# Kernel tuning notes

Hardware: AMD Instinct MI355X
Metric: run time of the kernel (lower is better)

Reference implementation:

```python
import jax, jax.numpy as jnp
import numpy as np

E = 768      # embedding_dim == hidden_dim (required for shape consistency)
U = 256      # number of utterances in the dialogue
NSPK = 8     # number of distinct speakers
SCALE = 0.03 # ~ torch's uniform(-1/sqrt(H), 1/sqrt(H)) init magnitude


def _p(k, shape):
    return jax.random.normal(k, shape, dtype=jnp.float32) * SCALE


def setup_inputs() -> dict:
    key = jax.random.key(0)
    ks = jax.random.split(key, 32)
    d = {}
    d["dialogue"] = jax.random.normal(ks[0], (U, E), dtype=jnp.float32)
    d["speakers"] = jax.random.randint(ks[1], (U,), 0, NSPK)
    # attention linears (stored [in, out], applied as x @ W + b)
    d["Wq"] = _p(ks[2], (E, E));      d["bq"] = _p(ks[3], (E,))
    d["Wk"] = _p(ks[4], (2 * E, E));  d["bk"] = _p(ks[5], (E,))
    d["Wv"] = _p(ks[6], (E, E));      d["bv"] = _p(ks[7], (E,))
    # speaker_GRU: input 2E, hidden E, bidirectional (torch layout [3H, in]/[3H, H])
    d["sWih_f"] = _p(ks[8], (3 * E, 2 * E)); d["sWhh_f"] = _p(ks[9], (3 * E, E))
    d["sbih_f"] = _p(ks[10], (3 * E,));      d["sbhh_f"] = _p(ks[11], (3 * E,))
    d["sWih_b"] = _p(ks[12], (3 * E, 2 * E)); d["sWhh_b"] = _p(ks[13], (3 * E, E))
    d["sbih_b"] = _p(ks[14], (3 * E,));       d["sbhh_b"] = _p(ks[15], (3 * E,))
    # global_GRU: input 3E, hidden E, bidirectional
    d["gWih_f"] = _p(ks[16], (3 * E, 3 * E)); d["gWhh_f"] = _p(ks[17], (3 * E, E))
    d["gbih_f"] = _p(ks[18], (3 * E,));       d["gbhh_f"] = _p(ks[19], (3 * E,))
    d["gWih_b"] = _p(ks[20], (3 * E, 3 * E)); d["gWhh_b"] = _p(ks[21], (3 * E, E))
    d["gbih_b"] = _p(ks[22], (3 * E,));       d["gbhh_b"] = _p(ks[23], (3 * E,))
    # random initial states, as in the original forward
    d["h0_global"] = jax.random.normal(ks[24], (2, E), dtype=jnp.float32)
    d["h0_speaker"] = jax.random.normal(ks[25], (2, E), dtype=jnp.float32)
    d["att0"] = jax.random.normal(ks[26], (E,), dtype=jnp.float32)
    return d


def _gru_cell(x, h, Wih, Whh, bih, bhh):
    # torch GRUCell math; gate order r, z, n
    gx = Wih @ x + bih
    gh = Whh @ h + bhh
    H = h.shape[0]
    r = jax.nn.sigmoid(gx[:H] + gh[:H])
    z = jax.nn.sigmoid(gx[H:2 * H] + gh[H:2 * H])
    n = jnp.tanh(gx[2 * H:] + r * gh[2 * H:])
    return (1.0 - z) * n + z * h


def reference(dialogue, speakers, Wq, bq, Wk, bk, Wv, bv,
              sWih_f, sWhh_f, sbih_f, sbhh_f, sWih_b, sWhh_b, sbih_b, sbhh_b,
              gWih_f, gWhh_f, gbih_f, gbhh_f, gWih_b, gWhh_b, gbih_b, gbhh_b,
              h0_global, h0_speaker, att0):
    Ul, El = dialogue.shape
    norm = jnp.sqrt(jnp.float32(El))
    pos = jnp.arange(Ul)
    sstates0 = jnp.broadcast_to(h0_speaker, (NSPK, 2, El))  # every speaker starts at h0_speaker
    buf0 = jnp.zeros((Ul, 2 * El), dtype=dialogue.dtype)    # global_output buffer

    def step(carry, xs):
        buf, gh, sst = carry
        u, sp, t = xs
        sh = sst[sp]  # [2, E] speaker hidden (fwd/bwd)
        # attention over global_output[:t+1] (row t is still zeros, as in torch)
        q = u @ Wq + bq                       # [E]
        k = buf @ Wk + bk                     # [U, E]
        v = k @ Wv + bv                       # [U, E] (note: w_v applied to projected key, as in source)
        score = (k @ q) / norm                # [U]
        score = jnp.where(pos <= t, score, jnp.float32(-1e9))
        att = jax.nn.softmax(score) @ v       # [E]
        att = jnp.where(t == 0, att0, att)    # t==0 uses random initial attention output
        tmp = jnp.concatenate([att, u])       # [2E]
        hf = _gru_cell(tmp, sh[0], sWih_f, sWhh_f, sbih_f, sbhh_f)
        hb = _gru_cell(tmp, sh[1], sWih_b, sWhh_b, sbih_b, sbhh_b)
        so = jnp.concatenate([hf, hb]) + tmp  # speaker_output[t] = GRU out + residual tmp
        sst = sst.at[sp].set(jnp.stack([hf, hb]))
        fop = jnp.concatenate([so, u])        # [3E]
        gf = _gru_cell(fop, gh[0], gWih_f, gWhh_f, gbih_f, gbhh_f)
        gb = _gru_cell(fop, gh[1], gWih_b, gWhh_b, gbih_b, gbhh_b)
        buf = buf.at[t].set(jnp.concatenate([gf, gb]))
        return (buf, jnp.stack([gf, gb]), sst), so

    (buf, _, _), so_seq = jax.lax.scan(step, (buf0, h0_global, sstates0),
                                       (dialogue, speakers, pos))
    return buf, so_seq  # (global_output [U,2E], speaker_output [U,2E])
```

## Files before the change

kernel.cpp:

```cpp
#include <hip/hip_runtime.h>
#include <hip/hip_bf16.h>

#define E_ 768
#define E2_ 1536
#define E3_ 2304
#define U_ 256
#define NORM_ 27.712812921102035f
#define NREP 16

typedef unsigned int u32;
typedef unsigned long long u64;

__device__ __align__(16) float g_Q[U_ * E_];
__device__ __align__(16) float g_WQg[U_ * E2_];
__device__ __align__(16) float g_WKVT[E_ * E2_];
__device__ __align__(16) float g_vb[E_];
__device__ int g_run;

__device__ __align__(64) u64 g_mb_bg[NREP * U_ * 8];
__device__ __align__(64) u64 g_mb_so[NREP * U_ * 8];
__device__ __align__(64) u64 g_mb_h [2 * NREP * U_ * 8 * 4];
__device__ __align__(64) u64 g_mb_sc[2 * NREP * U_];

__device__ __forceinline__ float bflo(u32 v){ return __uint_as_float(v << 16); }
__device__ __forceinline__ float bfhi(u32 v){ return __uint_as_float(v & 0xffff0000u); }

__device__ __forceinline__ u32 packbf(float lo, float hi){
  u32 a = __float_as_uint(lo), b = __float_as_uint(hi);
  a = (a + 0x7FFFu + ((a >> 16) & 1u)) >> 16;
  b = (b + 0x7FFFu + ((b >> 16) & 1u)) & 0xFFFF0000u;
  return (a & 0xFFFFu) | b;
}
__device__ __forceinline__ unsigned short bfr(float x){
  u32 a = __float_as_uint(x);
  return (unsigned short)((a + 0x7FFFu + ((a >> 16) & 1u)) >> 16);
}

__device__ __forceinline__ u64 aload64(const u64* p){
  return __hip_atomic_load(p, __ATOMIC_RELAXED, __HIP_MEMORY_SCOPE_AGENT);
}
__device__ __forceinline__ void astore64(u64* p, u64 v){
  __hip_atomic_store(p, v, __ATOMIC_RELAXED, __HIP_MEMORY_SCOPE_AGENT);
}
__device__ __forceinline__ u64 pk(float f, u32 tag){ return (u64)__float_as_uint(f) | ((u64)tag << 32); }
__device__ __forceinline__ float pf(u64 v){ return __uint_as_float((u32)v); }
__device__ __forceinline__ u32 ptag(u64 v){ return (u32)(v >> 32); }

__device__ __forceinline__ void bar_lds(){
  asm volatile("s_waitcnt lgkmcnt(0)\n\ts_barrier" ::: "memory");
}

__device__ __forceinline__ float wsum(float v){
#pragma unroll
  for (int o = 32; o > 0; o >>= 1) v += __shfl_xor(v, o, 64);
  return v;
}
__device__ __forceinline__ float wmax(float v){
#pragma unroll
  for (int o = 32; o > 0; o >>= 1) v = fmaxf(v, __shfl_xor(v, o, 64));
  return v;
}

__global__ __launch_bounds__(256) void init_kernel(const float* bk, const float* Wv,
                                                   const float* bv)
{
  __shared__ float acc4[4][64];
  int tid = threadIdx.x;
  if (blockIdx.x == 0 && tid == 0) g_run = g_run + 1;
  int b = blockIdx.x;
  int o = b * 64 + (tid & 63);
  int w = tid >> 6;
  float s = 0.f;
  for (int i2 = w * 192; i2 < w * 192 + 192; ++i2)
    s = fmaf(bk[i2], Wv[(size_t)i2 * E_ + o], s);
  acc4[w][tid & 63] = s;
  __syncthreads();
  if (w == 0)
    g_vb[o] = acc4[0][tid & 63] + acc4[1][tid & 63] + acc4[2][tid & 63] + acc4[3][tid & 63] + bv[o];
}

template<int ASRC, int BNK, int DST, int TC>
__global__ __launch_bounds__(256) void gemm32(const float* __restrict__ Aext, int lda,
                                              const float* __restrict__ B, int ldb,
                                              const float* __restrict__ bias, float scale,
                                              int ldc, int M, int N, int K)
{
  const float* A = (ASRC == 1) ? g_Q : Aext;
  float* C = (DST == 0) ? g_Q : (DST == 1) ? g_WQg : g_WKVT;
  __shared__ float As[64][17];
  __shared__ float Bs[16][65];
  int tid = threadIdx.x;
  int tx = tid & 15, ty = tid >> 4;
  int m0 = blockIdx.y * 64, n0 = blockIdx.x * 64;
  float acc[4][4] = {{0.f}};
  for (int k0 = 0; k0 < K; k0 += 16) {
#pragma unroll
    for (int i = 0; i < 4; ++i) {
      int li = tid + 256 * i;
      int m = li >> 4, kk = li & 15;
      As[m][kk] = A[(size_t)(m0 + m) * lda + k0 + kk];
    }
#pragma unroll
    for (int i = 0; i < 4; ++i) {
      int li = tid + 256 * i;
      if (BNK) {
        int n = li >> 4, kk = li & 15;
        Bs[kk][n] = B[(size_t)(n0 + n) * ldb + k0 + kk];
      } else {
        int kk = li >> 6, n = li & 63;
        Bs[kk][n] = B[(size_t)(k0 + kk) * ldb + n0 + n];
      }
    }
    __syncthreads();
#pragma unroll
    for (int kk = 0; kk < 16; ++kk) {
      float av[4], bv4[4];
#pragma unroll
      for (int i = 0; i < 4; ++i) av[i] = As[ty * 4 + i][kk];
#pragma unroll
      for (int j = 0; j < 4; ++j) bv4[j] = Bs[kk][tx * 4 + j];
#pragma unroll
      for (int i = 0; i < 4; ++i)
#pragma unroll
        for (int j = 0; j < 4; ++j) acc[i][j] = fmaf(av[i], bv4[j], acc[i][j]);
    }
    __syncthreads();
  }
#pragma unroll
  for (int i = 0; i < 4; ++i)
#pragma unroll
    for (int j = 0; j < 4; ++j) {
      int m = m0 + ty * 4 + i, n = n0 + tx * 4 + j;
      float c = acc[i][j] * scale;
      if (bias) c += bias[n];
      if (TC) C[(size_t)n * ldc + m] = c;
      else    C[(size_t)m * ldc + n] = c;
    }
}

struct SeqArgs {
  const float *dialogue, *sWih_f, *sWih_b, *sWhh_f, *sWhh_b,
      *sbih_f, *sbih_b, *sbhh_f, *sbhh_b,
      *gWih_f, *gWih_b, *gWhh_f, *gWhh_b, *gbih_f, *gbih_b, *gbhh_f, *gbhh_b,
      *att0, *h0g, *h0s;
  const int* speakers;
  float* out;
};

__global__ __launch_bounds__(256, 1) void seq_kernel(SeqArgs a)
{
  const int tid = threadIdx.x, wg = blockIdx.x;
  const int wave = tid >> 6, lane = tid & 63;
  const int h0 = wg * 3;
  const int myrep = wg & (NREP - 1);

  __shared__ float wsa[18][768];
  __shared__ float wkv_lds[3][E2_];
  __shared__ float M_l[18][U_];
  __shared__ float ghrow[E2_];
  __shared__ float bufc[E2_];
  __shared__ float hv[E2_];
  __shared__ float so_f[E2_];
  __shared__ float V_lds[U_][3];
  __shared__ float e_lds[U_];
  __shared__ float ghs_s[18], ghg_s[18], sxu[18], gxu[18], gxs[18], mcol[18];
  __shared__ float Mvb_l[18], A0_l[18];
  __shared__ float red4[4], red4b[4], pmax[4], pnum[4][4], att_s[3];
  __shared__ float pub12[12], pubbg[6];
  __shared__ float hloc[8][6];
  __shared__ float ghloc[6];
  __shared__ int spk_l[U_], locc_l[U_], pocc_l[U_];

  for (int idx = tid; idx < 18 * 768; idx += 256) {
    int r = idx / 768, e = idx - r * 768;
    int dir = r / 9, lr = r - dir * 9, g = lr / 3, d = lr - g * 3;
    int gr = g * E_ + h0 + d;
    const float* pa = (dir ? a.sWih_b : a.sWih_f) + (size_t)gr * E2_;
    wsa[r][e] = pa[e];
  }
  for (int idx = tid; idx < 3 * E2_; idx += 256) {
    int r = idx / E2_, k = idx - r * E2_;
    wkv_lds[r][k] = g_WKVT[(size_t)(h0 + r) * E2_ + k];
  }
  spk_l[tid] = a.speakers[tid] & 7;
  __syncthreads();
  {
    int mysp = spk_l[tid], lo = -1, cnt = 0;
    for (int s2 = 0; s2 <= tid; ++s2)
      if (spk_l[s2] == mysp) { cnt++; if (s2 < tid) lo = s2; }
    locc_l[tid] = lo;
    pocc_l[tid] = cnt & 1;
  }
#pragma unroll
  for (int q = 0; q < 5; ++q) {
    int sr = wave + 4 * q;
    if (sr < 18) {
      float s0 = 0.f, s1 = 0.f;
#pragma unroll
      for (int pp = 0; pp < 12; ++pp) {
        int e = lane + 64 * pp;
        float w = wsa[sr][e];
        s0 = fmaf(w, g_vb[e], s0);
        s1 = fmaf(w, a.att0[e], s1);
      }
      s0 = wsum(s0); s1 = wsum(s1);
      if (lane == 0) { Mvb_l[sr] = s0; A0_l[sr] = s1; }
    }
  }
  __syncthreads();
  for (int half = 0; half < 2; ++half) {
    float acc[9][6];
#pragma unroll
    for (int r = 0; r < 9; ++r)
#pragma unroll
      for (int c = 0; c < 6; ++c) acc[r][c] = 0.f;
    for (int e = 0; e < 768; e += 2) {
      const float* B0 = g_WKVT + (size_t)e * E2_ + tid;
      const float* B1 = B0 + E2_;
      float b0[6], b1[6];
#pragma unroll
      for (int c = 0; c < 6; ++c) { b0[c] = B0[256 * c]; b1[c] = B1[256 * c]; }
#pragma unroll
      for (int r = 0; r < 9; ++r) {
        float2 w = ((const float2*)wsa[half * 9 + r])[e >> 1];
#pragma unroll
        for (int c = 0; c < 6; ++c)
          acc[r][c] = fmaf(w.x, b0[c], fmaf(w.y, b1[c], acc[r][c]));
      }
    }
    __syncthreads();
    unsigned short* wsp = (unsigned short*)wsa;
#pragma unroll
    for (int r = 0; r < 9; ++r)
#pragma unroll
      for (int c = 0; c < 6; ++c)
        wsp[(half * 9 + r) * 1536 + tid + 256 * c] = bfr(acc[r][c]);
    __syncthreads();
  }
  const u32* wsp32 = (const u32*)wsa;

  u32 wSU[5][6], wSHH[5][6], wGHH[5][6], wGSO[5][12], wGU[5][6];
  float bSH[5], bGH[5], bSI[5], bGI[5];
#pragma unroll
  for (int q = 0; q < 5; ++q) {
    int sr = wave + 4 * q;
    if (sr < 18) {
      int dir = sr / 9, lr = sr - dir * 9, g = lr / 3, d = lr - g * 3;
      int gr = g * E_ + h0 + d;
      const float* pa  = (dir ? a.sWih_b : a.sWih_f) + (size_t)gr * E2_;
      const float* ph  = (dir ? a.sWhh_b : a.sWhh_f) + (size_t)gr * E_;
      const float* pgs = (dir ? a.gWih_b : a.gWih_f) + (size_t)gr * E3_;
      const float* pgh = (dir ? a.gWhh_b : a.gWhh_f) + (size_t)gr * E_;
#pragma unroll
      for (int pp = 0; pp < 6; ++pp) {
        int j2 = 2 * (lane + 64 * pp);
        wSU[q][pp]  = packbf(pa[768 + j2], pa[768 + j2 + 1]);
        wSHH[q][pp] = packbf(ph[j2], ph[j2 + 1]);
        wGHH[q][pp] = packbf(pgh[j2], pgh[j2 + 1]);
        wGU[q][pp]  = packbf(pgs[1536 + j2], pgs[1536 + j2 + 1]);
      }
#pragma unroll
      for (int pp = 0; pp < 12; ++pp) {
        int j2 = 2 * (lane + 64 * pp);
        wGSO[q][pp] = packbf(pgs[j2], pgs[j2 + 1]);
      }
      bSH[q] = (dir ? a.sbhh_b : a.sbhh_f)[gr];
      bSI[q] = (dir ? a.sbih_b : a.sbih_f)[gr];
      bGH[q] = (dir ? a.gbhh_b : a.gbhh_f)[gr];
      bGI[q] = (dir ? a.gbih_b : a.gbih_f)[gr];
    }
  }
  const float vb0 = g_vb[h0], vb1 = g_vb[h0 + 1], vb2 = g_vb[h0 + 2];
  if (tid < 6) ghloc[tid] = a.h0g[(tid / 3) * E_ + h0 + (tid % 3)];
  __syncthreads();

  const u32 rb = ((u32)g_run) << 9;

  for (int t = 0; t < U_; ++t) {
    const int sp = spk_l[t];
    const int locc = locc_l[t];
    const u32 tagT = rb + (u32)t;
    const float2* uv = (const float2*)(a.dialogue + (size_t)t * E_);

#pragma unroll
    for (int q = 0; q < 5; ++q) {
      int sr = wave + 4 * q;
      if (sr < 18) {
        float s3 = 0.f, s4 = 0.f;
#pragma unroll
        for (int pp = 0; pp < 6; ++pp) {
          int j = lane + 64 * pp;
          u32 v3 = wSU[q][pp], v4 = wGU[q][pp];
          float2 xu = uv[j];
          s3 = fmaf(bflo(v3), xu.x, s3); s3 = fmaf(bfhi(v3), xu.y, s3);
          s4 = fmaf(bflo(v4), xu.x, s4); s4 = fmaf(bfhi(v4), xu.y, s4);
        }
        s3 = wsum(s3); s4 = wsum(s4);
        if (lane == 0) { sxu[sr] = s3 + bSI[q]; gxu[sr] = s4 + bGI[q]; }
      }
    }

    float slp = 0.f;
    if (t == 0) {
      for (int i = tid; i < E2_; i += 256) ghrow[i] = a.h0g[i];
    } else {
      const u64* p = &g_mb_bg[((size_t)myrep * U_ + tid) * 8];
      u64 x0 = aload64(p), x1 = aload64(p + 1), x2 = aload64(p + 2);
      const u32 exp = rb + (u32)(t - 1);
      for (;;) {
        bool ok = (ptag(x0) == exp) & (ptag(x1) == exp) & (ptag(x2) == exp);
        if (ok) break;
        if (ptag(x0) != exp) x0 = aload64(p);
        if (ptag(x1) != exp) x1 = aload64(p + 1);
        if (ptag(x2) != exp) x2 = aload64(p + 2);
      }
      u32 w0 = (u32)x0, w1 = (u32)x1, w2 = (u32)x2;
      float f0 = bflo(w0), f1 = bfhi(w0), f2 = bflo(w1);
      float f3 = bfhi(w1), f4 = bflo(w2), f5 = bfhi(w2);
      ghrow[3 * tid]          = f0;
      ghrow[3 * tid + 1]      = f1;
      ghrow[3 * tid + 2]      = f2;
      ghrow[E_ + 3 * tid]     = f3;
      ghrow[E_ + 3 * tid + 1] = f4;
      ghrow[E_ + 3 * tid + 2] = f5;
      if (wg == t - 1) {
        bufc[3 * tid]          = f0;
        bufc[3 * tid + 1]      = f1;
        bufc[3 * tid + 2]      = f2;
        bufc[E_ + 3 * tid]     = f3;
        bufc[E_ + 3 * tid + 1] = f4;
        bufc[E_ + 3 * tid + 2] = f5;
      }
      const float* wq = g_WQg + (size_t)t * E2_;
      slp = f0 * wq[3 * tid] + f1 * wq[3 * tid + 1] + f2 * wq[3 * tid + 2]
          + f3 * wq[E_ + 3 * tid] + f4 * wq[E_ + 3 * tid + 1] + f5 * wq[E_ + 3 * tid + 2];
    }
    if (locc >= 0) {
      const int spar = pocc_l[t] ^ 1;
      const u64* p = &g_mb_h[((((size_t)spar * NREP + myrep) * U_ + tid) * 8 + sp) * 4];
      u64 x0 = aload64(p), x1 = aload64(p + 1), x2 = aload64(p + 2);
      const u32 exp = rb + (u32)locc;
      for (;;) {
        bool ok = (ptag(x0) == exp) & (ptag(x1) == exp) & (ptag(x2) == exp);
        if (ok) break;
        if (ptag(x0) != exp) x0 = aload64(p);
        if (ptag(x1) != exp) x1 = aload64(p + 1);
        if (ptag(x2) != exp) x2 = aload64(p + 2);
      }
      u32 w0 = (u32)x0, w1 = (u32)x1, w2 = (u32)x2;
      hv[3 * tid]          = bflo(w0);
      hv[3 * tid + 1]      = bfhi(w0);
      hv[3 * tid + 2]      = bflo(w1);
      hv[E_ + 3 * tid]     = bfhi(w1);
      hv[E_ + 3 * tid + 1] = bflo(w2);
      hv[E_ + 3 * tid + 2] = bfhi(w2);
    } else {
#pragma unroll
      for (int k = 0; k < 6; ++k) {
        int idx = (k / 3) * E_ + 3 * tid + (k % 3);
        hv[idx] = a.h0s[idx];
      }
    }
    slp = wsum(slp);
    if (lane == 0) red4[wave] = slp;
    bar_lds();

    if (t >= 1 && wg <= t - 1 && t + 1 < U_) {
      const float2* bc2 = (const float2*)bufc;
      const float2* wq2 = (const float2*)(g_WQg + (size_t)(t + 1) * E2_);
      float sb = 0.f;
#pragma unroll
      for (int pp = 0; pp < 3; ++pp) {
        int j = tid + 256 * pp;
        float2 x = bc2[j];
        float2 w = wq2[j];
        sb = fmaf(x.x, w.x, sb); sb = fmaf(x.y, w.y, sb);
      }
      sb = wsum(sb);
      if (lane == 0) red4b[wave] = sb;
    }
#pragma unroll
    for (int q = 0; q < 5; ++q) {
      int sr = wave + 4 * q;
      if (sr < 18) {
        int dir = sr / 9;
        const float2* hv2 = (const float2*)hv + dir * 384;
        const float2* gv2 = (const float2*)ghrow + dir * 384;
        const float2* gf  = (const float2*)ghrow;
        const u32* wrow = wsp32 + (size_t)sr * 768;
        float s1 = 0.f, s2 = 0.f, sm = 0.f;
#pragma unroll
        for (int pp = 0; pp < 6; ++pp) {
          int j = lane + 64 * pp;
          u32 v1 = wSHH[q][pp], v2 = wGHH[q][pp];
          float2 xh = hv2[j];
          float2 xg = gv2[j];
          s1 = fmaf(bflo(v1), xh.x, s1); s1 = fmaf(bfhi(v1), xh.y, s1);
          s2 = fmaf(bflo(v2), xg.x, s2); s2 = fmaf(bfhi(v2), xg.y, s2);
        }
#pragma unroll
        for (int pp = 0; pp < 12; ++pp) {
          int j = lane + 64 * pp;
          u32 v = wrow[j];
          float2 x = gf[j];
          sm = fmaf(bflo(v), x.x, sm); sm = fmaf(bfhi(v), x.y, sm);
        }
        s1 = wsum(s1); s2 = wsum(s2); sm = wsum(sm);
        if (lane == 0) {
          ghs_s[sr] = s1 + bSH[q];
          ghg_s[sr] = s2 + bGH[q];
          mcol[sr]  = sm + Mvb_l[sr];
        }
      }
    }
    if (t >= 1 && wave < 3) {
      const float2* gr2 = (const float2*)ghrow;
      const float2* kv2 = (const float2*)wkv_lds[wave];
      float s = 0.f;
#pragma unroll
      for (int pp = 0; pp < 12; ++pp) {
        int j = lane + 64 * pp;
        float2 x = gr2[j];
        float2 wv = kv2[j];
        s = fmaf(wv.x, x.x, s);
        s = fmaf(wv.y, x.y, s);
      }
      s = wsum(s);
      if (lane == 0)
        V_lds[t - 1][wave] = s + (wave == 0 ? vb0 : (wave == 1 ? vb1 : vb2));
    }
    bar_lds();
    if (t >= 1 && wg <= t - 1 && t + 1 < U_ && tid < NREP)
      astore64(&g_mb_sc[((size_t)((t + 1) & 1) * NREP + tid) * U_ + wg],
               pk(red4b[0] + red4b[1] + red4b[2] + red4b[3], rb + (u32)(t + 1)));

    if (t == 0) {
      if (tid < 18) gxs[tid] = A0_l[tid];
      if (tid < 3) att_s[tid] = a.att0[h0 + tid];
      bar_lds();
    } else {
      float sc;
      if (tid <= t - 2) {
        const u64* p = &g_mb_sc[((size_t)(t & 1) * NREP + myrep) * U_ + tid];
        u64 x = aload64(p);
        while (ptag(x) != tagT) x = aload64(p);
        sc = pf(x);
      } else if (tid == t - 1) {
        sc = red4[0] + red4[1] + red4[2] + red4[3];
      } else sc = (tid == t) ? 0.f : -3.0e38f;
      float m = wmax(sc);
      if (lane == 0) pmax[wave] = m;
      bar_lds();
      float mall = fmaxf(fmaxf(pmax[0], pmax[1]), fmaxf(pmax[2], pmax[3]));
      float e = 0.f, n0 = 0.f, n1 = 0.f, n2 = 0.f;
      if (tid <= t) {
        e = expf(sc - mall);
        if (tid < t) { n0 = e * V_lds[tid][0]; n1 = e * V_lds[tid][1]; n2 = e * V_lds[tid][2]; }
        else         { n0 = e * vb0; n1 = e * vb1; n2 = e * vb2; }
      }
      e_lds[tid] = e;
      float es = wsum(e); n0 = wsum(n0); n1 = wsum(n1); n2 = wsum(n2);
      if (lane == 0) { pnum[wave][0] = es; pnum[wave][1] = n0; pnum[wave][2] = n1; pnum[wave][3] = n2; }
      bar_lds();
      float den = pnum[0][0] + pnum[1][0] + pnum[2][0] + pnum[3][0];
      if (tid < 3) {
        float nn = pnum[0][tid + 1] + pnum[1][tid + 1] + pnum[2][tid + 1] + pnum[3][tid + 1];
        att_s[tid] = nn / den;
      }
#pragma unroll
      for (int q = 0; q < 5; ++q) {
        int sr = wave + 4 * q;
        if (sr < 18) {
          float dm = 0.f;
#pragma unroll
          for (int pp = 0; pp < 4; ++pp) {
            int j = lane + 64 * pp;
            dm += (j <= t - 2) ? e_lds[j] * M_l[sr][j] : 0.f;
          }
          dm = wsum(dm);
          if (lane == 0) {
            float mc = mcol[sr];
            gxs[sr] = (dm + e_lds[t - 1] * mc + e_lds[t] * Mvb_l[sr]) / den;
            M_l[sr][t - 1] = mc;
          }
        }
      }
      bar_lds();
    }

    if (tid < 6) {
      int dir = tid / 3, d = tid - dir * 3, h = h0 + d;
      float xr = gxs[dir * 9 + d]     + sxu[dir * 9 + d];
      float xz = gxs[dir * 9 + 3 + d] + sxu[dir * 9 + 3 + d];
      float xn = gxs[dir * 9 + 6 + d] + sxu[dir * 9 + 6 + d];
      float hr = ghs_s[dir * 9 + d], hz = ghs_s[dir * 9 + 3 + d], hn = ghs_s[dir * 9 + 6 + d];
      float hp = (locc >= 0) ? hloc[sp][tid] : a.h0s[dir * E_ + h];
      float r = 1.f / (1.f + expf(-(xr + hr)));
      float z = 1.f / (1.f + expf(-(xz + hz)));
      float n = tanhf(xn + r * hn);
      float hnew = (1.f - z) * n + z * hp;
      float resid = dir ? a.dialogue[(size_t)t * E_ + h] : att_s[d];
      float so = hnew + resid;
      hloc[sp][tid] = hnew;
      pub12[tid] = hnew; pub12[6 + tid] = so;
      a.out[(size_t)U_ * E2_ + (size_t)t * E2_ + dir * E_ + h] = so;
    }
    bar_lds();
    if (tid < 48) {
      int rep = tid & 15, slot = tid >> 4;
      u32 pay = packbf(pub12[6 + 2 * slot], pub12[7 + 2 * slot]);
      astore64(&g_mb_so[((size_t)rep * U_ + wg) * 8 + slot], (u64)pay | ((u64)tagT << 32));
    } else if (tid < 96) {
      int k = tid - 48, rep = k & 15, slot = k >> 4;
      u32 pay = packbf(pub12[2 * slot], pub12[1 + 2 * slot]);
      astore64(&g_mb_h[((((size_t)pocc_l[t] * NREP + rep) * U_ + wg) * 8 + sp) * 4 + slot],
               (u64)pay | ((u64)tagT << 32));
    }

    {
      const u64* p = &g_mb_so[((size_t)myrep * U_ + tid) * 8];
      u64 x0 = aload64(p), x1 = aload64(p + 1), x2 = aload64(p + 2);
      for (;;) {
        bool ok = (ptag(x0) == tagT) & (ptag(x1) == tagT) & (ptag(x2) == tagT);
        if (ok) break;
        if (ptag(x0) != tagT) x0 = aload64(p);
        if (ptag(x1) != tagT) x1 = aload64(p + 1);
        if (ptag(x2) != tagT) x2 = aload64(p + 2);
      }
      u32 w0 = (u32)x0, w1 = (u32)x1, w2 = (u32)x2;
      so_f[3 * tid]          = bflo(w0);
      so_f[3 * tid + 1]      = bfhi(w0);
      so_f[3 * tid + 2]      = bflo(w1);
      so_f[E_ + 3 * tid]     = bfhi(w1);
      so_f[E_ + 3 * tid + 1] = bflo(w2);
      so_f[E_ + 3 * tid + 2] = bfhi(w2);
    }
    bar_lds();
#pragma unroll
    for (int q = 0; q < 5; ++q) {
      int sr = wave + 4 * q;
      if (sr < 18) {
        const float2* so2 = (const float2*)so_f;
        float s = 0.f;
#pragma unroll
        for (int pp = 0; pp < 12; ++pp) {
          int j = lane + 64 * pp;
          u32 v = wGSO[q][pp];
          float2 x = so2[j];
          s = fmaf(bflo(v), x.x, s); s = fmaf(bfhi(v), x.y, s);
        }
        s = wsum(s);
        if (lane == 0) gxs[sr] = s;
      }
    }
    bar_lds();
    if (tid < 6) {
      int dir = tid / 3, d = tid - dir * 3, h = h0 + d;
      float xr = gxs[dir * 9 + d]     + gxu[dir * 9 + d];
      float xz = gxs[dir * 9 + 3 + d] + gxu[dir * 9 + 3 + d];
      float xn = gxs[dir * 9 + 6 + d] + gxu[dir * 9 + 6 + d];
      float hr = ghg_s[dir * 9 + d], hz = ghg_s[dir * 9 + 3 + d], hn = ghg_s[dir * 9 + 6 + d];
      float hp = ghloc[tid];
      float r = 1.f / (1.f + expf(-(xr + hr)));
      float z = 1.f / (1.f + expf(-(xz + hz)));
      float n = tanhf(xn + r * hn);
      float hnew = (1.f - z) * n + z * hp;
      ghloc[tid] = hnew;
      pubbg[tid] = hnew;
      a.out[(size_t)t * E2_ + dir * E_ + h] = hnew;
    }
    bar_lds();
    if (tid < 48) {
      int rep = tid & 15, slot = tid >> 4;
      u32 pay = packbf(pubbg[2 * slot], pubbg[2 * slot + 1]);
      astore64(&g_mb_bg[((size_t)rep * U_ + wg) * 8 + slot], (u64)pay | ((u64)tagT << 32));
    }
  }
}

extern "C" void kernel_launch(void* const* d_in, const int* in_sizes, int n_in,
                              void* d_out, int out_size, void* d_ws, size_t ws_size,
                              hipStream_t stream)
{
  (void)in_sizes; (void)n_in; (void)out_size; (void)d_ws; (void)ws_size;
  const float* dialogue = (const float*)d_in[0];
  const int* speakers = (const int*)d_in[1];
  const float* Wq = (const float*)d_in[2];
  const float* bq = (const float*)d_in[3];
  const float* Wk = (const float*)d_in[4];
  const float* bk = (const float*)d_in[5];
  const float* Wv = (const float*)d_in[6];
  const float* bv = (const float*)d_in[7];
  const float* sWih_f = (const float*)d_in[8];
  const float* sWhh_f = (const float*)d_in[9];
  const float* sbih_f = (const float*)d_in[10];
  const float* sbhh_f = (const float*)d_in[11];
  const float* sWih_b = (const float*)d_in[12];
  const float* sWhh_b = (const float*)d_in[13];
  const float* sbih_b = (const float*)d_in[14];
  const float* sbhh_b = (const float*)d_in[15];
  const float* gWih_f = (const float*)d_in[16];
  const float* gWhh_f = (const float*)d_in[17];
  const float* gbih_f = (const float*)d_in[18];
  const float* gbhh_f = (const float*)d_in[19];
  const float* gWih_b = (const float*)d_in[20];
  const float* gWhh_b = (const float*)d_in[21];
  const float* gbih_b = (const float*)d_in[22];
  const float* gbhh_b = (const float*)d_in[23];
  const float* h0_global = (const float*)d_in[24];
  const float* h0_speaker = (const float*)d_in[25];
  const float* att0 = (const float*)d_in[26];

  init_kernel<<<dim3(12), dim3(256), 0, stream>>>(bk, Wv, bv);

  gemm32<0, 0, 0, 0><<<dim3(12, 4), dim3(256), 0, stream>>>(
      dialogue, 768, Wq, 768, bq, 1.f, 768, 256, 768, 768);
  gemm32<1, 1, 1, 0><<<dim3(24, 4), dim3(256), 0, stream>>>(
      nullptr, 768, Wk, 768, nullptr, 1.f / NORM_, 1536, 256, 1536, 768);
  gemm32<0, 0, 2, 1><<<dim3(12, 24), dim3(256), 0, stream>>>(
      Wk, 768, Wv, 768, nullptr, 1.f, 1536, 1536, 768, 768);

  SeqArgs args;
  args.dialogue = dialogue;
  args.sWih_f = sWih_f; args.sWih_b = sWih_b; args.sWhh_f = sWhh_f; args.sWhh_b = sWhh_b;
  args.sbih_f = sbih_f; args.sbih_b = sbih_b; args.sbhh_f = sbhh_f; args.sbhh_b = sbhh_b;
  args.gWih_f = gWih_f; args.gWih_b = gWih_b; args.gWhh_f = gWhh_f; args.gWhh_b = gWhh_b;
  args.gbih_f = gbih_f; args.gbih_b = gbih_b; args.gbhh_f = gbhh_f; args.gbhh_b = gbhh_b;
  args.att0 = att0; args.h0g = h0_global; args.h0s = h0_speaker;
  args.speakers = speakers;
  args.out = (float*)d_out;

  seq_kernel<<<dim3(256), dim3(256), 0, stream>>>(args);
}
```

Measured before the change: 5.049 ms.

## Precompute next-step attention partial softmax off the critical path

Restructures the per-step schedule so the attention softmax over earlier scores (t-1 and older) is computed at the end of the previous step, after the global GRU publish. The current step then only merges the two newest terms using an online-softmax rescale. The next-step dialogue input projections and the WQ row prefetch into LDS are also moved into the slack after the speaker publish, with double-buffered gxu. The aim is to shorten the serial critical path between cross-workgroup mailbox waits, at the cost of more barriers and LDS use plus the need for correct handling of the new ordering.

```diff
diff --git a/kernel.cpp b/kernel.cpp
--- a/kernel.cpp
+++ b/kernel.cpp
@@ -161,11 +161,14 @@
   __shared__ float bufc[E2_];
   __shared__ float hv[E2_];
   __shared__ float so_f[E2_];
+  __shared__ float wq_lds[E2_];
   __shared__ float V_lds[U_][3];
   __shared__ float e_lds[U_];
-  __shared__ float ghs_s[18], ghg_s[18], sxu[18], gxu[18], gxs[18], mcol[18];
-  __shared__ float Mvb_l[18], A0_l[18];
+  __shared__ float ghs_s[18], ghg_s[18], sxu[18], gxs[18], mcol[18];
+  __shared__ float gxu2[2][18];
+  __shared__ float Mvb_l[18], A0_l[18], Mdotp[18];
   __shared__ float red4[4], red4b[4], pmax[4], pnum[4][4], att_s[3];
+  __shared__ float mpart_s, denp_s, npart_s[3];
   __shared__ float pub12[12], pubbg[6];
   __shared__ float hloc[8][6];
   __shared__ float ghloc[6];
@@ -274,31 +277,33 @@
   if (tid < 6) ghloc[tid] = a.h0g[(tid / 3) * E_ + h0 + (tid % 3)];
   __syncthreads();
 
+  {
+    const float2* uv0 = (const float2*)a.dialogue;
+#pragma unroll
+    for (int q = 0; q < 5; ++q) {
+      int sr = wave + 4 * q;
+      if (sr < 18) {
+        float s3 = 0.f, s4 = 0.f;
+#pragma unroll
+        for (int pp = 0; pp < 6; ++pp) {
+          int j = lane + 64 * pp;
+          u32 v3 = wSU[q][pp], v4 = wGU[q][pp];
+          float2 xu = uv0[j];
+          s3 = fmaf(bflo(v3), xu.x, s3); s3 = fmaf(bfhi(v3), xu.y, s3);
+          s4 = fmaf(bflo(v4), xu.x, s4); s4 = fmaf(bfhi(v4), xu.y, s4);
+        }
+        s3 = wsum(s3); s4 = wsum(s4);
+        if (lane == 0) { sxu[sr] = s3 + bSI[q]; gxu2[0][sr] = s4 + bGI[q]; }
+      }
+    }
+  }
+
   const u32 rb = ((u32)g_run) << 9;
 
   for (int t = 0; t < U_; ++t) {
     const int sp = spk_l[t];
     const int locc = locc_l[t];
     const u32 tagT = rb + (u32)t;
-    const float2* uv = (const float2*)(a.dialogue + (size_t)t * E_);
-
-#pragma unroll
-    for (int q = 0; q < 5; ++q) {
-      int sr = wave + 4 * q;
-      if (sr < 18) {
-        float s3 = 0.f, s4 = 0.f;
-#pragma unroll
-        for (int pp = 0; pp < 6; ++pp) {
-          int j = lane + 64 * pp;
-          u32 v3 = wSU[q][pp], v4 = wGU[q][pp];
-          float2 xu = uv[j];
-          s3 = fmaf(bflo(v3), xu.x, s3); s3 = fmaf(bfhi(v3), xu.y, s3);
-          s4 = fmaf(bflo(v4), xu.x, s4); s4 = fmaf(bfhi(v4), xu.y, s4);
-        }
-        s3 = wsum(s3); s4 = wsum(s4);
-        if (lane == 0) { sxu[sr] = s3 + bSI[q]; gxu[sr] = s4 + bGI[q]; }
-      }
-    }
 
     float slp = 0.f;
     if (t == 0) {
@@ -331,9 +336,9 @@
         bufc[E_ + 3 * tid + 1] = f4;
         bufc[E_ + 3 * tid + 2] = f5;
       }
-      const float* wq = g_WQg + (size_t)t * E2_;
-      slp = f0 * wq[3 * tid] + f1 * wq[3 * tid + 1] + f2 * wq[3 * tid + 2]
-          + f3 * wq[E_ + 3 * tid] + f4 * wq[E_ + 3 * tid + 1] + f5 * wq[E_ + 3 * tid + 2];
+      slp = f0 * wq_lds[3 * tid] + f1 * wq_lds[3 * tid + 1] + f2 * wq_lds[3 * tid + 2]
+          + f3 * wq_lds[E_ + 3 * tid] + f4 * wq_lds[E_ + 3 * tid + 1]
+          + f5 * wq_lds[E_ + 3 * tid + 2];
     }
     if (locc >= 0) {
       const int spar = pocc_l[t] ^ 1;
@@ -365,20 +370,6 @@
     if (lane == 0) red4[wave] = slp;
     bar_lds();
 
-    if (t >= 1 && wg <= t - 1 && t + 1 < U_) {
-      const float2* bc2 = (const float2*)bufc;
-      const float2* wq2 = (const float2*)(g_WQg + (size_t)(t + 1) * E2_);
-      float sb = 0.f;
-#pragma unroll
-      for (int pp = 0; pp < 3; ++pp) {
-        int j = tid + 256 * pp;
-        float2 x = bc2[j];
-        float2 w = wq2[j];
-        sb = fmaf(x.x, w.x, sb); sb = fmaf(x.y, w.y, sb);
-      }
-      sb = wsum(sb);
-      if (lane == 0) red4b[wave] = sb;
-    }
 #pragma unroll
     for (int q = 0; q < 5; ++q) {
       int sr = wave + 4 * q;
@@ -409,7 +400,9 @@
         if (lane == 0) {
           ghs_s[sr] = s1 + bSH[q];
           ghg_s[sr] = s2 + bGH[q];
-          mcol[sr]  = sm + Mvb_l[sr];
+          float mc = sm + Mvb_l[sr];
+          mcol[sr] = mc;
+          if (t >= 1) M_l[sr][t - 1] = mc;
         }
       }
     }
@@ -430,63 +423,27 @@
         V_lds[t - 1][wave] = s + (wave == 0 ? vb0 : (wave == 1 ? vb1 : vb2));
     }
     bar_lds();
-    if (t >= 1 && wg <= t - 1 && t + 1 < U_ && tid < NREP)
-      astore64(&g_mb_sc[((size_t)((t + 1) & 1) * NREP + tid) * U_ + wg],
-               pk(red4b[0] + red4b[1] + red4b[2] + red4b[3], rb + (u32)(t + 1)));
 
     if (t == 0) {
       if (tid < 18) gxs[tid] = A0_l[tid];
       if (tid < 3) att_s[tid] = a.att0[h0 + tid];
-      bar_lds();
     } else {
-      float sc;
-      if (tid <= t - 2) {
-        const u64* p = &g_mb_sc[((size_t)(t & 1) * NREP + myrep) * U_ + tid];
-        u64 x = aload64(p);
-        while (ptag(x) != tagT) x = aload64(p);
-        sc = pf(x);
-      } else if (tid == t - 1) {
-        sc = red4[0] + red4[1] + red4[2] + red4[3];
-      } else sc = (tid == t) ? 0.f : -3.0e38f;
-      float m = wmax(sc);
-      if (lane == 0) pmax[wave] = m;
-      bar_lds();
-      float mall = fmaxf(fmaxf(pmax[0], pmax[1]), fmaxf(pmax[2], pmax[3]));
-      float e = 0.f, n0 = 0.f, n1 = 0.f, n2 = 0.f;
-      if (tid <= t) {
-        e = expf(sc - mall);
-        if (tid < t) { n0 = e * V_lds[tid][0]; n1 = e * V_lds[tid][1]; n2 = e * V_lds[tid][2]; }
-        else         { n0 = e * vb0; n1 = e * vb1; n2 = e * vb2; }
-      }
-      e_lds[tid] = e;
-      float es = wsum(e); n0 = wsum(n0); n1 = wsum(n1); n2 = wsum(n2);
-      if (lane == 0) { pnum[wave][0] = es; pnum[wave][1] = n0; pnum[wave][2] = n1; pnum[wave][3] = n2; }
-      bar_lds();
-      float den = pnum[0][0] + pnum[1][0] + pnum[2][0] + pnum[3][0];
-      if (tid < 3) {
-        float nn = pnum[0][tid + 1] + pnum[1][tid + 1] + pnum[2][tid + 1] + pnum[3][tid + 1];
-        att_s[tid] = nn / den;
-      }
-#pragma unroll
-      for (int q = 0; q < 5; ++q) {
-        int sr = wave + 4 * q;
-        if (sr < 18) {
-          float dm = 0.f;
-#pragma unroll
-          for (int pp = 0; pp < 4; ++pp) {
-            int j = lane + 64 * pp;
-            dm += (j <= t - 2) ? e_lds[j] * M_l[sr][j] : 0.f;
-          }
-          dm = wsum(dm);
-          if (lane == 0) {
-            float mc = mcol[sr];
-            gxs[sr] = (dm + e_lds[t - 1] * mc + e_lds[t] * Mvb_l[sr]) / den;
-            M_l[sr][t - 1] = mc;
-          }
-        }
-      }
-      bar_lds();
-    }
+      if (tid < 18) {
+        float slpT = red4[0] + red4[1] + red4[2] + red4[3];
+        float mp = mpart_s;
+        float mall = fmaxf(fmaxf(mp, slpT), 0.f);
+        float al = expf(mp - mall);
+        float e1 = expf(slpT - mall);
+        float e0 = expf(-mall);
+        float den = al * denp_s + e1 + e0;
+        gxs[tid] = (al * Mdotp[tid] + e1 * mcol[tid] + e0 * Mvb_l[tid]) / den;
+        if (tid < 3) {
+          float vbd = (tid == 0) ? vb0 : ((tid == 1) ? vb1 : vb2);
+          att_s[tid] = (al * npart_s[tid] + e1 * V_lds[t - 1][tid] + e0 * vbd) / den;
+        }
+      }
+    }
+    bar_lds();
 
     if (tid < 6) {
       int dir = tid / 3, d = tid - dir * 3, h = h0 + d;
@@ -517,6 +474,49 @@
                (u64)pay | ((u64)tagT << 32));
     }
 
+    if (t + 1 < U_) {
+      const float2* uvn = (const float2*)(a.dialogue + (size_t)(t + 1) * E_);
+#pragma unroll
+      for (int q = 0; q < 5; ++q) {
+        int sr = wave + 4 * q;
+        if (sr < 18) {
+          float s3 = 0.f, s4 = 0.f;
+#pragma unroll
+          for (int pp = 0; pp < 6; ++pp) {
+            int j = lane + 64 * pp;
+            u32 v3 = wSU[q][pp], v4 = wGU[q][pp];
+            float2 xu = uvn[j];
+            s3 = fmaf(bflo(v3), xu.x, s3); s3 = fmaf(bfhi(v3), xu.y, s3);
+            s4 = fmaf(bflo(v4), xu.x, s4); s4 = fmaf(bfhi(v4), xu.y, s4);
+          }
+          s3 = wsum(s3); s4 = wsum(s4);
+          if (lane == 0) { sxu[sr] = s3 + bSI[q]; gxu2[(t + 1) & 1][sr] = s4 + bGI[q]; }
+        }
+      }
+      if (wg <= t - 1) {
+        const float2* bc2 = (const float2*)bufc;
+        const float2* wq2 = (const float2*)(g_WQg + (size_t)(t + 1) * E2_);
+        float sb = 0.f;
+#pragma unroll
+        for (int pp = 0; pp < 3; ++pp) {
+          int j = tid + 256 * pp;
+          float2 x = bc2[j];
+          float2 w = wq2[j];
+          sb = fmaf(x.x, w.x, sb); sb = fmaf(x.y, w.y, sb);
+        }
+        sb = wsum(sb);
+        if (lane == 0) red4b[wave] = sb;
+      }
+      {
+        const float* wn = g_WQg + (size_t)(t + 1) * E2_;
+        for (int i = tid; i < E2_; i += 256) wq_lds[i] = wn[i];
+      }
+    }
+    bar_lds();
+    if (t >= 1 && wg <= t - 1 && t + 1 < U_ && tid < NREP)
+      astore64(&g_mb_sc[((size_t)((t + 1) & 1) * NREP + tid) * U_ + wg],
+               pk(red4b[0] + red4b[1] + red4b[2] + red4b[3], rb + (u32)(t + 1)));
+
     {
       const u64* p = &g_mb_so[((size_t)myrep * U_ + tid) * 8];
       u64 x0 = aload64(p), x1 = aload64(p + 1), x2 = aload64(p + 2);
@@ -556,9 +556,9 @@
     bar_lds();
     if (tid < 6) {
       int dir = tid / 3, d = tid - dir * 3, h = h0 + d;
-      float xr = gxs[dir * 9 + d]     + gxu[dir * 9 + d];
-      float xz = gxs[dir * 9 + 3 + d] + gxu[dir * 9 + 3 + d];
-      float xn = gxs[dir * 9 + 6 + d] + gxu[dir * 9 + 6 + d];
+      float xr = gxs[dir * 9 + d]     + gxu2[t & 1][dir * 9 + d];
+      float xz = gxs[dir * 9 + 3 + d] + gxu2[t & 1][dir * 9 + 3 + d];
+      float xn = gxs[dir * 9 + 6 + d] + gxu2[t & 1][dir * 9 + 6 + d];
       float hr = ghg_s[dir * 9 + d], hz = ghg_s[dir * 9 + 3 + d], hn = ghg_s[dir * 9 + 6 + d];
       float hp = ghloc[tid];
       float r = 1.f / (1.f + expf(-(xr + hr)));
@@ -574,6 +574,50 @@
       int rep = tid & 15, slot = tid >> 4;
       u32 pay = packbf(pubbg[2 * slot], pubbg[2 * slot + 1]);
       astore64(&g_mb_bg[((size_t)rep * U_ + wg) * 8 + slot], (u64)pay | ((u64)tagT << 32));
+    }
+
+    if (t + 1 < U_) {
+      float sc2;
+      if (tid <= t - 1) {
+        const u64* p = &g_mb_sc[((size_t)((t + 1) & 1) * NREP + myrep) * U_ + tid];
+        u64 x = aload64(p);
+        const u32 expn = rb + (u32)(t + 1);
+        while (ptag(x) != expn) x = aload64(p);
+        sc2 = pf(x);
+      } else sc2 = -3.0e38f;
+      float m = wmax(sc2);
+      if (lane == 0) pmax[wave] = m;
+      bar_lds();
+      float mp = fmaxf(fmaxf(pmax[0], pmax[1]), fmaxf(pmax[2], pmax[3]));
+      float e = 0.f, q0 = 0.f, q1 = 0.f, q2 = 0.f;
+      if (tid <= t - 1) {
+        e = expf(sc2 - mp);
+        q0 = e * V_lds[tid][0]; q1 = e * V_lds[tid][1]; q2 = e * V_lds[tid][2];
+      }
+      e_lds[tid] = e;
+      float es = wsum(e); q0 = wsum(q0); q1 = wsum(q1); q2 = wsum(q2);
+      if (lane == 0) { pnum[wave][0] = es; pnum[wave][1] = q0; pnum[wave][2] = q1; pnum[wave][3] = q2; }
+      bar_lds();
+      if (tid == 0) {
+        mpart_s = mp;
+        denp_s = pnum[0][0] + pnum[1][0] + pnum[2][0] + pnum[3][0];
+      }
+      if (tid < 3)
+        npart_s[tid] = pnum[0][tid + 1] + pnum[1][tid + 1] + pnum[2][tid + 1] + pnum[3][tid + 1];
+#pragma unroll
+      for (int q = 0; q < 5; ++q) {
+        int sr = wave + 4 * q;
+        if (sr < 18) {
+          float dm = 0.f;
+#pragma unroll
+          for (int pp = 0; pp < 4; ++pp) {
+            int j = lane + 64 * pp;
+            dm += (j <= t - 1) ? e_lds[j] * M_l[sr][j] : 0.f;
+          }
+          dm = wsum(dm);
+          if (lane == 0) Mdotp[sr] = dm;
+        }
+      }
     }
   }
 }
```

Result: faster. 4.916 ms (-2.6%).
